# Optimization experiments

Hardware: AMD Instinct MI355X
Metric: run time of the kernel (lower is better)

Reference implementation:

```python
import jax, jax.numpy as jnp
import numpy as np

D_MODEL = 1024
N_HEADS = 16
HEAD_DIM = D_MODEL // N_HEADS
B, T = 2, 2048


def _rotate_half(x):
    # Faithful to module's _apply_rotary: view (..., D//2, 2), pair -> (-x1, x0)
    xr = x.reshape(*x.shape[:-1], HEAD_DIM // 2, 2)
    rot = jnp.stack([-xr[..., 1], xr[..., 0]], axis=-1)
    return rot.reshape(*x.shape)


def setup_inputs() -> dict:
    key = jax.random.key(0)
    ks = jax.random.split(key, 9)
    s = 1.0 / np.sqrt(D_MODEL)
    return {
        "x": jax.random.normal(ks[0], (B, T, D_MODEL), jnp.float32),
        "Wq": jax.random.normal(ks[1], (D_MODEL, D_MODEL), jnp.float32) * s,
        "bq": jax.random.normal(ks[2], (D_MODEL,), jnp.float32) * 0.02,
        "Wk": jax.random.normal(ks[3], (D_MODEL, D_MODEL), jnp.float32) * s,
        "bk": jax.random.normal(ks[4], (D_MODEL,), jnp.float32) * 0.02,
        "Wv": jax.random.normal(ks[5], (D_MODEL, D_MODEL), jnp.float32) * s,
        "bv": jax.random.normal(ks[6], (D_MODEL,), jnp.float32) * 0.02,
        "Wo": jax.random.normal(ks[7], (D_MODEL, D_MODEL), jnp.float32) * s,
        "bo": jax.random.normal(ks[8], (D_MODEL,), jnp.float32) * 0.02,
    }


def reference(x, Wq, bq, Wk, bk, Wv, bv, Wo, bo):
    b, t, _ = x.shape
    # QKV projections (nn.Linear: x @ W.T + b), split heads -> (B, H, T, Dh)
    def proj(W, bias):
        y = x @ W.T + bias
        return y.reshape(b, t, N_HEADS, HEAD_DIM).transpose(0, 2, 1, 3)

    q = _rotate_half(proj(Wq, bq))
    k = _rotate_half(proj(Wk, bk))
    v = proj(Wv, bv)

    scale = 1.0 / jnp.sqrt(jnp.asarray(HEAD_DIM, x.dtype))
    scores = jnp.einsum('bhqd,bhkd->bhqk', q, k) * scale
    causal = jnp.tril(jnp.ones((t, t), bool))  # (T, T)
    scores = jnp.where(causal, scores, jnp.asarray(-jnp.inf, scores.dtype))
    attn = jax.nn.softmax(scores, axis=-1)
    out = jnp.einsum('bhqk,bhkd->bhqd', attn, v)
    out = out.transpose(0, 2, 1, 3).reshape(b, t, D_MODEL)
    return out @ Wo.T + bo
```

## Files before the change

kernel.cpp:

```cpp
#include <hip/hip_runtime.h>
#include <stdint.h>

#define DM 1024
#define NH 16
#define HD 64
#define BB 2
#define TT 2048
#define MT (BB*TT)

typedef __bf16 bfrag __attribute__((ext_vector_type(8)));
typedef float  f32x4 __attribute__((ext_vector_type(4)));

__device__ __forceinline__ unsigned short f2bf(float f) {
  union { float f; unsigned u; } v; v.f = f;
  unsigned r = v.u + 0x7fffu + ((v.u >> 16) & 1u);
  return (unsigned short)(r >> 16);
}

__device__ __forceinline__ unsigned short f2bf_hw(float f) {
  __bf16 b = (__bf16)f;
  union { __bf16 b; unsigned short u; } v; v.b = b;
  return v.u;
}

__device__ __forceinline__ unsigned int pack2bf(float a, float b) {
  union { __bf16 h[2]; unsigned int u; } v;
  v.h[0] = (__bf16)a; v.h[1] = (__bf16)b;
  return v.u;
}

__device__ __forceinline__ void async16(const void* g, void* l) {
  __builtin_amdgcn_global_load_lds(
      (const __attribute__((address_space(1))) unsigned int*)g,
      (__attribute__((address_space(3))) unsigned int*)l, 16, 0, 0);
}

__global__ __launch_bounds__(256) void cvt_kernel(
    const float* __restrict__ x,  const float* __restrict__ Wq,
    const float* __restrict__ Wk, const float* __restrict__ Wv,
    const float* __restrict__ Wo,
    unsigned short* __restrict__ xb, unsigned short* __restrict__ wqkv,
    unsigned short* __restrict__ wob) {
  int i = blockIdx.x * 256 + threadIdx.x;
  const int NX = MT * DM / 4;
  const int NW = DM * DM / 4;
  const float* src; unsigned short* dst; int off;
  if      (i < NX)        { src = x;  dst = xb;              off = i; }
  else if (i < NX + NW)   { src = Wq; dst = wqkv;            off = i - NX; }
  else if (i < NX + 2*NW) { src = Wk; dst = wqkv + DM*DM;    off = i - NX - NW; }
  else if (i < NX + 3*NW) { src = Wv; dst = wqkv + 2*DM*DM;  off = i - NX - 2*NW; }
  else                    { src = Wo; dst = wob;             off = i - NX - 3*NW; }
  float4 v = ((const float4*)src)[off];
  ushort4 o;
  o.x = f2bf(v.x); o.y = f2bf(v.y); o.z = f2bf(v.z); o.w = f2bf(v.w);
  ((ushort4*)dst)[off] = o;
}

template<int EPI, int TM>
__global__ __launch_bounds__(256) void gemm_bt(
    const unsigned short* __restrict__ A, const unsigned short* __restrict__ Bm,
    const float* __restrict__ bias0, const float* __restrict__ bias1,
    const float* __restrict__ bias2,
    unsigned short* __restrict__ Qo, unsigned short* __restrict__ Ko,
    unsigned short* __restrict__ Vo, float* __restrict__ Co) {
  constexpr int WM = TM / 2;
  constexpr int MI = WM / 16;
  const int tid = threadIdx.x;
  const int wave = tid >> 6, lane = tid & 63;
  const int lr = lane & 15, quad = lane >> 4;
  const int m0 = blockIdx.y * TM, n0 = blockIdx.x * 128;
  __shared__ __align__(16) unsigned short sA[2][TM * 32];
  __shared__ __align__(16) unsigned short sB[2][128 * 32];
  const f32x4 zero = {0.f, 0.f, 0.f, 0.f};
  f32x4 acc[MI][4];
#pragma unroll
  for (int i = 0; i < MI; i++)
#pragma unroll
    for (int j = 0; j < 4; j++) acc[i][j] = zero;
  const int wm = (wave >> 1) * WM, wn = (wave & 1) * 64;

  auto stage = [&](int kt, int buf) {
    const int k0 = kt * 32;
#pragma unroll
    for (int rep = 0; rep < TM / 64; ++rep) {
      int fb = rep * 2048 + wave * 512;
      int fl = fb + lane * 8;
      int row = fl >> 5;
      int c   = (fl >> 3) & 3;
      int col = ((c ^ ((row >> 1) & 3)) << 3);
      async16(A + (size_t)(m0 + row) * 1024 + k0 + col, &sA[buf][fb]);
    }
#pragma unroll
    for (int rep = 0; rep < 2; ++rep) {
      int fb = rep * 2048 + wave * 512;
      int fl = fb + lane * 8;
      int row = fl >> 5;
      int c   = (fl >> 3) & 3;
      int col = ((c ^ ((row >> 1) & 3)) << 3);
      async16(Bm + (size_t)(n0 + row) * 1024 + k0 + col, &sB[buf][fb]);
    }
  };

  stage(0, 0);
  for (int kt = 0; kt < 32; ++kt) {
    const int buf = kt & 1;
    __syncthreads();
    if (kt + 1 < 32) stage(kt + 1, buf ^ 1);
    bfrag af[MI], bfr[4];
#pragma unroll
    for (int i = 0; i < MI; i++) {
      int ra = wm + i * 16 + lr;
      af[i]  = *(const bfrag*)&sA[buf][ra * 32 + ((quad ^ ((ra >> 1) & 3)) << 3)];
    }
#pragma unroll
    for (int j = 0; j < 4; j++) {
      int rb = wn + j * 16 + lr;
      bfr[j] = *(const bfrag*)&sB[buf][rb * 32 + ((quad ^ ((rb >> 1) & 3)) << 3)];
    }
#pragma unroll
    for (int i = 0; i < MI; i++)
#pragma unroll
      for (int j = 0; j < 4; j++)
        acc[i][j] = __builtin_amdgcn_mfma_f32_16x16x32_bf16(af[i], bfr[j], acc[i][j], 0, 0, 0);
  }

  if (EPI == 0) {
#pragma unroll
    for (int j = 0; j < 4; j++) {
      int n = n0 + wn + j * 16 + lr;
      int qkv = n >> 10, nn = n & 1023;
      float bias = (qkv == 0 ? bias0 : qkv == 1 ? bias1 : bias2)[nn];
      int h = nn >> 6, d = nn & 63;
      if (qkv == 2) {
#pragma unroll
        for (int i = 0; i < MI; i++) {
          int t0 = m0 + wm + i * 16 + quad * 4;
          int b = t0 >> 11, tt = t0 & 2047;
          size_t bb = (size_t)((b << 4) + h) * (TT * 64);
          int kk0 = tt & 63;
          size_t off = bb + (size_t)(tt >> 6) * 4096 +
                       (size_t)((kk0 >> 3) << 9) + (d << 3) + (kk0 & 7);
          ushort4 pk;
          pk.x = f2bf(acc[i][j][0] + bias);
          pk.y = f2bf(acc[i][j][1] + bias);
          pk.z = f2bf(acc[i][j][2] + bias);
          pk.w = f2bf(acc[i][j][3] + bias);
          *(ushort4*)(Vo + off) = pk;
        }
      } else {
#pragma unroll
        for (int i = 0; i < MI; i++)
#pragma unroll
          for (int r = 0; r < 4; r++) {
            int m = m0 + wm + i * 16 + quad * 4 + r;
            float vb = acc[i][j][r] + bias;
            float pv = __shfl_xor(vb, 1);
            float val = (n & 1) ? pv : -pv;
            int b = m >> 11, t = m & 2047;
            size_t base = (size_t)((b << 4) + h) * (TT * 64);
            if (qkv == 0) {
              Qo[base + (size_t)t * 64 + d] = f2bf(val * 0.125f);
            } else {
              int kk = t & 63;
              size_t off = base + (size_t)(t >> 6) * 4096 +
                           (size_t)((d >> 3) << 9) + (kk << 3) + (d & 7);
              Ko[off] = f2bf(val);
            }
          }
      }
    }
  } else {
#pragma unroll
    for (int j = 0; j < 4; j++) {
      int n = n0 + wn + j * 16 + lr;
      float bias = bias0[n];
#pragma unroll
      for (int i = 0; i < MI; i++)
#pragma unroll
        for (int r = 0; r < 4; r++) {
          int m = m0 + wm + i * 16 + quad * 4 + r;
          Co[(size_t)m * 1024 + n] = acc[i][j][r] + bias;
        }
    }
  }
}

__global__ __launch_bounds__(256, 2) void flash_kernel(
    const unsigned short* __restrict__ Qg, const unsigned short* __restrict__ Kg,
    const unsigned short* __restrict__ Vg, unsigned short* __restrict__ Og) {
  const int p = blockIdx.x;
  const int bh = blockIdx.y;
  const int tid = threadIdx.x, wave = tid >> 6, lane = tid & 63;
  const int lr = lane & 15, quad = lane >> 4;
  __shared__ __align__(16) unsigned short sK[2][4096];
  __shared__ __align__(16) unsigned short sV[2][4096];
  __shared__ __align__(16) unsigned short sP[4][1024];
  const size_t base = (size_t)bh * (TT * 64);
  const int qtA = p, qtB = 31 - p;
  const int nA = p + 1, nB = 32 - p;
  const int qgA = qtA * 64 + wave * 16 + lr;
  const int qgB = qtB * 64 + wave * 16 + lr;
  const f32x4 zero = {0.f, 0.f, 0.f, 0.f};

  bfrag qA0, qA1, qB0, qB1;
  {
    const unsigned short* qr = Qg + base + (size_t)qgA * 64;
    qA0 = *(const bfrag*)(qr + quad * 8);
    qA1 = *(const bfrag*)(qr + 32 + quad * 8);
  }
  {
    const unsigned short* qr = Qg + base + (size_t)qgB * 64;
    qB0 = *(const bfrag*)(qr + quad * 8);
    qB1 = *(const bfrag*)(qr + 32 + quad * 8);
  }
  f32x4 oA[4], oB[4];
  float rsA = 0.f, rsB = 0.f;
#pragma unroll
  for (int j = 0; j < 4; j++) { oA[j] = zero; oB[j] = zero; }

  const unsigned short* kgb = Kg + base;
  const unsigned short* vgb = Vg + base;

#pragma unroll
  for (int rep = 0; rep < 2; ++rep) {
    int fb = rep * 2048 + wave * 512;
    async16(kgb + fb + lane * 8, &sK[0][fb]);
    async16(vgb + fb + lane * 8, &sV[0][fb]);
  }

  bfrag vf0[4], vf1[4];

  auto process = [&](const f32x4 (&sT)[4], f32x4 (&o)[4], float& rs,
                     int qg, bool diag, int kb) {
    unsigned short* sPw = sP[wave];
#pragma unroll
    for (int ct = 0; ct < 4; ++ct) {
      float e[4];
#pragma unroll
      for (int r = 0; r < 4; ++r)
        e[r] = __expf(sT[ct][r] - 11.0f);
      if (diag) {
#pragma unroll
        for (int r = 0; r < 4; ++r) {
          int key = kb + ct * 16 + quad * 4 + r;
          if (key > qg) e[r] = 0.f;
        }
      }
      rs += (e[0] + e[1]) + (e[2] + e[3]);
      uint2 w;
      w.x = pack2bf(e[0], e[1]);
      w.y = pack2bf(e[2], e[3]);
      *(uint2*)&sPw[(ct * 2 + (quad >> 1)) * 128 + lr * 8 + (quad & 1) * 4] = w;
    }
    bfrag pf0 = *(const bfrag*)&sPw[quad * 128 + lr * 8];
    bfrag pf1 = *(const bfrag*)&sPw[(4 + quad) * 128 + lr * 8];
#pragma unroll
    for (int j = 0; j < 4; j++) {
      o[j] = __builtin_amdgcn_mfma_f32_16x16x32_bf16(vf0[j], pf0, o[j], 0, 0, 0);
      o[j] = __builtin_amdgcn_mfma_f32_16x16x32_bf16(vf1[j], pf1, o[j], 0, 0, 0);
    }
  };

  for (int kt = 0; kt < nB; ++kt) {
    const int buf = kt & 1;
    __syncthreads();
    if (kt + 1 < nB) {
#pragma unroll
      for (int rep = 0; rep < 2; ++rep) {
        int fb = rep * 2048 + wave * 512;
        const size_t g = (size_t)(kt + 1) * 4096 + fb + lane * 8;
        async16(kgb + g, &sK[buf ^ 1][fb]);
        async16(vgb + g, &sV[buf ^ 1][fb]);
      }
    }
    bfrag kf0[4], kf1[4];
#pragma unroll
    for (int j = 0; j < 4; j++) {
      int row8 = (j * 16 + lr) * 8;
      kf0[j] = *(const bfrag*)&sK[buf][quad * 512 + row8];
      kf1[j] = *(const bfrag*)&sK[buf][(4 + quad) * 512 + row8];
      vf0[j] = *(const bfrag*)&sV[buf][quad * 512 + row8];
      vf1[j] = *(const bfrag*)&sV[buf][(4 + quad) * 512 + row8];
    }
    const bool doA = (kt < nA);
    f32x4 sTB[4], sTA[4];
#pragma unroll
    for (int ct = 0; ct < 4; ct++) {
      f32x4 t = __builtin_amdgcn_mfma_f32_16x16x32_bf16(kf0[ct], qB0, zero, 0, 0, 0);
      sTB[ct] = __builtin_amdgcn_mfma_f32_16x16x32_bf16(kf1[ct], qB1, t,    0, 0, 0);
    }
    if (doA) {
#pragma unroll
      for (int ct = 0; ct < 4; ct++) {
        f32x4 t = __builtin_amdgcn_mfma_f32_16x16x32_bf16(kf0[ct], qA0, zero, 0, 0, 0);
        sTA[ct] = __builtin_amdgcn_mfma_f32_16x16x32_bf16(kf1[ct], qA1, t,    0, 0, 0);
      }
    }
    process(sTB, oB, rsB, qgB, kt == nB - 1, kt * 64);
    if (doA) process(sTA, oA, rsA, qgA, kt == nA - 1, kt * 64);
  }

  rsA += __shfl_xor(rsA, 16); rsA += __shfl_xor(rsA, 32);
  rsB += __shfl_xor(rsB, 16); rsB += __shfl_xor(rsB, 32);
  const float invA = 1.0f / rsA, invB = 1.0f / rsB;

  const int b = bh >> 4, h = bh & 15;
#pragma unroll
  for (int j = 0; j < 4; j++) {
    ushort4 pa, pb;
    pa.x = f2bf_hw(oA[j][0] * invA); pa.y = f2bf_hw(oA[j][1] * invA);
    pa.z = f2bf_hw(oA[j][2] * invA); pa.w = f2bf_hw(oA[j][3] * invA);
    pb.x = f2bf_hw(oB[j][0] * invB); pb.y = f2bf_hw(oB[j][1] * invB);
    pb.z = f2bf_hw(oB[j][2] * invB); pb.w = f2bf_hw(oB[j][3] * invB);
    int col = h * 64 + j * 16 + quad * 4;
    *(ushort4*)(Og + (size_t)(b * TT + qgA) * 1024 + col) = pa;
    *(ushort4*)(Og + (size_t)(b * TT + qgB) * 1024 + col) = pb;
  }
}

extern "C" void kernel_launch(void* const* d_in, const int* in_sizes, int n_in,
                              void* d_out, int out_size, void* d_ws, size_t ws_size,
                              hipStream_t stream) {
  const float* x  = (const float*)d_in[0];
  const float* Wq = (const float*)d_in[1];
  const float* bq = (const float*)d_in[2];
  const float* Wk = (const float*)d_in[3];
  const float* bk = (const float*)d_in[4];
  const float* Wv = (const float*)d_in[5];
  const float* bv = (const float*)d_in[6];
  const float* Wo = (const float*)d_in[7];
  const float* bo = (const float*)d_in[8];
  float* out = (float*)d_out;

  unsigned short* ws = (unsigned short*)d_ws;
  unsigned short* xb   = ws;
  unsigned short* wqkv = ws + (size_t)4 * 1024 * 1024;
  unsigned short* wob  = ws + (size_t)7 * 1024 * 1024;
  unsigned short* Qb   = ws + (size_t)8 * 1024 * 1024;
  unsigned short* Kb   = ws + (size_t)12 * 1024 * 1024;
  unsigned short* Vb   = ws + (size_t)16 * 1024 * 1024;
  unsigned short* Ob   = ws + (size_t)20 * 1024 * 1024;

  cvt_kernel<<<dim3(8192), dim3(256), 0, stream>>>(x, Wq, Wk, Wv, Wo, xb, wqkv, wob);
  gemm_bt<0, 128><<<dim3(24, 32), dim3(256), 0, stream>>>(xb, wqkv, bq, bk, bv,
                                                          Qb, Kb, Vb, (float*)nullptr);
  flash_kernel<<<dim3(16, 32), dim3(256), 0, stream>>>(Qb, Kb, Vb, Ob);
  gemm_bt<1, 64><<<dim3(8, 64), dim3(256), 0, stream>>>(Ob, wob, bo, nullptr, nullptr,
                                                        nullptr, nullptr, nullptr, out);
}
```

Measured before the change: 205.5 us.

## Precompute LDS/global addresses and interleave A/B softmax and PV MFMAs in flash

The GEMM moves per-iteration address and swizzle computation into pointers computed once and advanced each step, and unrolls the k-loop by two so buffer indices are compile-time constants. The flash kernel enlarges the per-wave P scratch so both query tiles' probabilities can be written before any are read. Their PV MFMAs are then interleaved, so the two independent accumulation chains can overlap. This adds LDS usage in flash, which could affect occupancy.

```diff
diff --git a/kernel.cpp b/kernel.cpp
--- a/kernel.cpp
+++ b/kernel.cpp
@@ -65,6 +65,7 @@
     unsigned short* __restrict__ Vo, float* __restrict__ Co) {
   constexpr int WM = TM / 2;
   constexpr int MI = WM / 16;
+  constexpr int AR = TM / 64;
   const int tid = threadIdx.x;
   const int wave = tid >> 6, lane = tid & 63;
   const int lr = lane & 15, quad = lane >> 4;
@@ -79,49 +80,63 @@
     for (int j = 0; j < 4; j++) acc[i][j] = zero;
   const int wm = (wave >> 1) * WM, wn = (wave & 1) * 64;
 
-  auto stage = [&](int kt, int buf) {
-    const int k0 = kt * 32;
-#pragma unroll
-    for (int rep = 0; rep < TM / 64; ++rep) {
-      int fb = rep * 2048 + wave * 512;
-      int fl = fb + lane * 8;
-      int row = fl >> 5;
-      int c   = (fl >> 3) & 3;
-      int col = ((c ^ ((row >> 1) & 3)) << 3);
-      async16(A + (size_t)(m0 + row) * 1024 + k0 + col, &sA[buf][fb]);
-    }
-#pragma unroll
-    for (int rep = 0; rep < 2; ++rep) {
-      int fb = rep * 2048 + wave * 512;
-      int fl = fb + lane * 8;
-      int row = fl >> 5;
-      int c   = (fl >> 3) & 3;
-      int col = ((c ^ ((row >> 1) & 3)) << 3);
-      async16(Bm + (size_t)(n0 + row) * 1024 + k0 + col, &sB[buf][fb]);
-    }
-  };
-
-  stage(0, 0);
-  for (int kt = 0; kt < 32; ++kt) {
-    const int buf = kt & 1;
+  const unsigned short* gA[AR];
+  const unsigned short* gB[2];
+#pragma unroll
+  for (int rep = 0; rep < AR; ++rep) {
+    int fl = rep * 2048 + wave * 512 + lane * 8;
+    int row = fl >> 5, c = (fl >> 3) & 3;
+    gA[rep] = A + (size_t)(m0 + row) * 1024 + ((c ^ ((row >> 1) & 3)) << 3);
+  }
+#pragma unroll
+  for (int rep = 0; rep < 2; ++rep) {
+    int fl = rep * 2048 + wave * 512 + lane * 8;
+    int row = fl >> 5, c = (fl >> 3) & 3;
+    gB[rep] = Bm + (size_t)(n0 + row) * 1024 + ((c ^ ((row >> 1) & 3)) << 3);
+  }
+  const int offA = (wm + lr) * 32 + ((quad ^ ((lr >> 1) & 3)) << 3);
+  const int offB = (wn + lr) * 32 + ((quad ^ ((lr >> 1) & 3)) << 3);
+  const unsigned short* aB_[2] = { &sA[0][offA], &sA[1][offA] };
+  const unsigned short* bB_[2] = { &sB[0][offB], &sB[1][offB] };
+
+#pragma unroll
+  for (int rep = 0; rep < AR; ++rep)
+    async16(gA[rep], &sA[0][rep * 2048 + wave * 512]);
+#pragma unroll
+  for (int rep = 0; rep < 2; ++rep)
+    async16(gB[rep], &sB[0][rep * 2048 + wave * 512]);
+
+  auto kstep = [&](int buf, bool dostage) {
     __syncthreads();
-    if (kt + 1 < 32) stage(kt + 1, buf ^ 1);
+    if (dostage) {
+#pragma unroll
+      for (int rep = 0; rep < AR; ++rep) {
+        gA[rep] += 32;
+        async16(gA[rep], &sA[buf ^ 1][rep * 2048 + wave * 512]);
+      }
+#pragma unroll
+      for (int rep = 0; rep < 2; ++rep) {
+        gB[rep] += 32;
+        async16(gB[rep], &sB[buf ^ 1][rep * 2048 + wave * 512]);
+      }
+    }
+    const unsigned short* ab = aB_[buf];
+    const unsigned short* bb = bB_[buf];
     bfrag af[MI], bfr[4];
 #pragma unroll
-    for (int i = 0; i < MI; i++) {
-      int ra = wm + i * 16 + lr;
-      af[i]  = *(const bfrag*)&sA[buf][ra * 32 + ((quad ^ ((ra >> 1) & 3)) << 3)];
-    }
-#pragma unroll
-    for (int j = 0; j < 4; j++) {
-      int rb = wn + j * 16 + lr;
-      bfr[j] = *(const bfrag*)&sB[buf][rb * 32 + ((quad ^ ((rb >> 1) & 3)) << 3)];
-    }
+    for (int i = 0; i < MI; i++) af[i] = *(const bfrag*)(ab + i * 512);
+#pragma unroll
+    for (int j = 0; j < 4; j++)  bfr[j] = *(const bfrag*)(bb + j * 512);
 #pragma unroll
     for (int i = 0; i < MI; i++)
 #pragma unroll
       for (int j = 0; j < 4; j++)
         acc[i][j] = __builtin_amdgcn_mfma_f32_16x16x32_bf16(af[i], bfr[j], acc[i][j], 0, 0, 0);
+  };
+
+  for (int it = 0; it < 16; ++it) {
+    kstep(0, true);
+    kstep(1, it < 15);
   }
 
   if (EPI == 0) {
@@ -194,7 +209,7 @@
   const int lr = lane & 15, quad = lane >> 4;
   __shared__ __align__(16) unsigned short sK[2][4096];
   __shared__ __align__(16) unsigned short sV[2][4096];
-  __shared__ __align__(16) unsigned short sP[4][1024];
+  __shared__ __align__(16) unsigned short sP[4][2048];
   const size_t base = (size_t)bh * (TT * 64);
   const int qtA = p, qtB = 31 - p;
   const int nA = p + 1, nB = 32 - p;
@@ -228,38 +243,10 @@
     async16(vgb + fb + lane * 8, &sV[0][fb]);
   }
 
-  bfrag vf0[4], vf1[4];
-
-  auto process = [&](const f32x4 (&sT)[4], f32x4 (&o)[4], float& rs,
-                     int qg, bool diag, int kb) {
-    unsigned short* sPw = sP[wave];
-#pragma unroll
-    for (int ct = 0; ct < 4; ++ct) {
-      float e[4];
-#pragma unroll
-      for (int r = 0; r < 4; ++r)
-        e[r] = __expf(sT[ct][r] - 11.0f);
-      if (diag) {
-#pragma unroll
-        for (int r = 0; r < 4; ++r) {
-          int key = kb + ct * 16 + quad * 4 + r;
-          if (key > qg) e[r] = 0.f;
-        }
-      }
-      rs += (e[0] + e[1]) + (e[2] + e[3]);
-      uint2 w;
-      w.x = pack2bf(e[0], e[1]);
-      w.y = pack2bf(e[2], e[3]);
-      *(uint2*)&sPw[(ct * 2 + (quad >> 1)) * 128 + lr * 8 + (quad & 1) * 4] = w;
-    }
-    bfrag pf0 = *(const bfrag*)&sPw[quad * 128 + lr * 8];
-    bfrag pf1 = *(const bfrag*)&sPw[(4 + quad) * 128 + lr * 8];
-#pragma unroll
-    for (int j = 0; j < 4; j++) {
-      o[j] = __builtin_amdgcn_mfma_f32_16x16x32_bf16(vf0[j], pf0, o[j], 0, 0, 0);
-      o[j] = __builtin_amdgcn_mfma_f32_16x16x32_bf16(vf1[j], pf1, o[j], 0, 0, 0);
-    }
-  };
+  const int fro = quad * 512 + lr * 8;
+  unsigned short* sPw = sP[wave];
+  const int pwr = lr * 8 + (quad & 1) * 4;
+  const int pq2 = quad >> 1;
 
   for (int kt = 0; kt < nB; ++kt) {
     const int buf = kt & 1;
@@ -273,14 +260,15 @@
         async16(vgb + g, &sV[buf ^ 1][fb]);
       }
     }
-    bfrag kf0[4], kf1[4];
+    const unsigned short* kb = &sK[buf][fro];
+    const unsigned short* vb = &sV[buf][fro];
+    bfrag kf0[4], kf1[4], vf0[4], vf1[4];
 #pragma unroll
     for (int j = 0; j < 4; j++) {
-      int row8 = (j * 16 + lr) * 8;
-      kf0[j] = *(const bfrag*)&sK[buf][quad * 512 + row8];
-      kf1[j] = *(const bfrag*)&sK[buf][(4 + quad) * 512 + row8];
-      vf0[j] = *(const bfrag*)&sV[buf][quad * 512 + row8];
-      vf1[j] = *(const bfrag*)&sV[buf][(4 + quad) * 512 + row8];
+      kf0[j] = *(const bfrag*)(kb + j * 128);
+      kf1[j] = *(const bfrag*)(kb + 2048 + j * 128);
+      vf0[j] = *(const bfrag*)(vb + j * 128);
+      vf1[j] = *(const bfrag*)(vb + 2048 + j * 128);
     }
     const bool doA = (kt < nA);
     f32x4 sTB[4], sTA[4];
@@ -296,8 +284,56 @@
         sTA[ct] = __builtin_amdgcn_mfma_f32_16x16x32_bf16(kf1[ct], qA1, t,    0, 0, 0);
       }
     }
-    process(sTB, oB, rsB, qgB, kt == nB - 1, kt * 64);
-    if (doA) process(sTA, oA, rsA, qgA, kt == nA - 1, kt * 64);
+    const bool diagB = (kt == nB - 1), diagA = (kt == nA - 1);
+#pragma unroll
+    for (int ct = 0; ct < 4; ++ct) {
+      float e[4];
+#pragma unroll
+      for (int r = 0; r < 4; ++r) e[r] = __expf(sTB[ct][r] - 11.0f);
+      if (diagB) {
+#pragma unroll
+        for (int r = 0; r < 4; ++r)
+          if (kt * 64 + ct * 16 + quad * 4 + r > qgB) e[r] = 0.f;
+      }
+      rsB += (e[0] + e[1]) + (e[2] + e[3]);
+      uint2 w; w.x = pack2bf(e[0], e[1]); w.y = pack2bf(e[2], e[3]);
+      *(uint2*)&sPw[(ct * 2 + pq2) * 128 + pwr] = w;
+    }
+    if (doA) {
+#pragma unroll
+      for (int ct = 0; ct < 4; ++ct) {
+        float e[4];
+#pragma unroll
+        for (int r = 0; r < 4; ++r) e[r] = __expf(sTA[ct][r] - 11.0f);
+        if (diagA) {
+#pragma unroll
+          for (int r = 0; r < 4; ++r)
+            if (kt * 64 + ct * 16 + quad * 4 + r > qgA) e[r] = 0.f;
+        }
+        rsA += (e[0] + e[1]) + (e[2] + e[3]);
+        uint2 w; w.x = pack2bf(e[0], e[1]); w.y = pack2bf(e[2], e[3]);
+        *(uint2*)&sPw[1024 + (ct * 2 + pq2) * 128 + pwr] = w;
+      }
+    }
+    bfrag pfB0 = *(const bfrag*)&sPw[quad * 128 + lr * 8];
+    bfrag pfB1 = *(const bfrag*)&sPw[(4 + quad) * 128 + lr * 8];
+    if (doA) {
+      bfrag pfA0 = *(const bfrag*)&sPw[1024 + quad * 128 + lr * 8];
+      bfrag pfA1 = *(const bfrag*)&sPw[1024 + (4 + quad) * 128 + lr * 8];
+#pragma unroll
+      for (int j = 0; j < 4; j++) {
+        oB[j] = __builtin_amdgcn_mfma_f32_16x16x32_bf16(vf0[j], pfB0, oB[j], 0, 0, 0);
+        oA[j] = __builtin_amdgcn_mfma_f32_16x16x32_bf16(vf0[j], pfA0, oA[j], 0, 0, 0);
+        oB[j] = __builtin_amdgcn_mfma_f32_16x16x32_bf16(vf1[j], pfB1, oB[j], 0, 0, 0);
+        oA[j] = __builtin_amdgcn_mfma_f32_16x16x32_bf16(vf1[j], pfA1, oA[j], 0, 0, 0);
+      }
+    } else {
+#pragma unroll
+      for (int j = 0; j < 4; j++) {
+        oB[j] = __builtin_amdgcn_mfma_f32_16x16x32_bf16(vf0[j], pfB0, oB[j], 0, 0, 0);
+        oB[j] = __builtin_amdgcn_mfma_f32_16x16x32_bf16(vf1[j], pfB1, oB[j], 0, 0, 0);
+      }
+    }
   }
 
   rsA += __shfl_xor(rsA, 16); rsA += __shfl_xor(rsA, 32);
```

New measurement: 211.8 us. 1.03x slower.
